# Kernel tuning notes

Measured on AMD Instinct MI355X. Metric: run time of the kernel, lower is better.

The kernel has to match this reference:

```python
import jax, jax.numpy as jnp
import numpy as np

B, S, E, F = 64, 8192, 8, 32  # batch, seq, embed_dim(=n_qubits), ffn_dim


def setup_inputs() -> dict:
    key = jax.random.key(0)
    k_x, k_t, k_w1, k_b1, k_w2, k_b2 = jax.random.split(key, 6)
    x = jax.random.normal(k_x, (B, S, E), dtype=jnp.float32)
    theta = jax.random.normal(k_t, (E,), dtype=jnp.float32)  # trainable RX angles
    lim1 = 1.0 / np.sqrt(E)
    lim2 = 1.0 / np.sqrt(F)
    w1 = jax.random.uniform(k_w1, (E, F), jnp.float32, -lim1, lim1)
    b1 = jax.random.uniform(k_b1, (F,), jnp.float32, -lim1, lim1)
    w2 = jax.random.uniform(k_w2, (F, E), jnp.float32, -lim2, lim2)
    b2 = jax.random.uniform(k_b2, (E,), jnp.float32, -lim2, lim2)
    return {"x": x, "theta": theta, "w1": w1, "b1": b1, "w2": w2, "b2": b2}


def reference(x, theta, w1, b1, w2, b2):
    # Quantum circuit: per wire i, RX(x_i) then RX(theta_i) on |0>, measure PauliZ.
    # Single-qubit RX gates compose: <Z> after RX(phi)|0> = cos(phi). Wires are
    # independent (no entangling gates), so MeasureAll(PauliZ) = cos(x + theta).
    q_out = jnp.cos(x + theta)                      # [B, S, E]
    h = jax.nn.relu(q_out @ w1 + b1)                # [B, S, F]
    return h @ w2 + b2                              # [B, S, E]
```

## Files before the change

kernel.cpp:

```cpp
#include <hip/hip_runtime.h>


#define TPB 256

typedef _Float16 h8  __attribute__((ext_vector_type(8)));
typedef __fp16   fp16x2 __attribute__((ext_vector_type(2)));
typedef float    f4  __attribute__((ext_vector_type(4)));
typedef float    f16v __attribute__((ext_vector_type(16)));

union H2I { fp16x2 h; int i; };
union I4H8 { int i[4]; h8 h; };

__device__ __forceinline__ int pack_f16(float a, float b) {
    H2I u;
    u.h = __builtin_amdgcn_cvt_pkrtz(a, b);
    return u.i;
}

__global__ __launch_bounds__(TPB) void ffq_kernel(
    const float4* __restrict__ xv,
    const float*  __restrict__ theta,
    const float*  __restrict__ w1,
    const float*  __restrict__ b1,
    const float*  __restrict__ w2,
    const float*  __restrict__ b2,
    float4*       __restrict__ outv,
    int ntile, int nwaves)
{
    __shared__ int lds[4 * 576];

    const int tid  = threadIdx.x;
    const int lane = tid & 63;
    const int widx = tid >> 6;
    const int half = lane >> 5;
    const int l31  = lane & 31;
    const int quad = (lane >> 4) & 3;
    const int m16  = lane & 15;

    h8 a1;
#pragma unroll
    for (int j = 0; j < 8; ++j)
        a1[j] = (half == 0) ? (_Float16)w1[j * 32 + l31] : (_Float16)0;

    h8 a2;
#pragma unroll
    for (int j = 0; j < 8; ++j)
        a2[j] = (m16 < 8) ? (_Float16)w2[(quad * 8 + j) * 8 + m16] : (_Float16)0;

    f16v c10;
#pragma unroll
    for (int r = 0; r < 16; ++r)
        c10[r] = b1[(r & 3) + 8 * (r >> 2) + 4 * half];

    f4 c20;
#pragma unroll
    for (int r = 0; r < 4; ++r)
        c20[r] = (quad < 2) ? b2[quad * 4 + r] : 0.0f;

    float th[8];
#pragma unroll
    for (int e = 0; e < 8; ++e) th[e] = theta[e];

    const int base_w = widx * 576;
    const int wid = blockIdx.x * (TPB / 64) + widx;

    float4 curA = make_float4(0.f, 0.f, 0.f, 0.f);
    float4 curC = curA;
    if (wid < ntile && half == 0) {
        const int tok = wid * 32 + l31;
        curA = xv[2 * tok];
        curC = xv[2 * tok + 1];
    }

    for (int tile = wid; tile < ntile; tile += nwaves) {
        float4 nA = curA, nC = curC;
        const int nxt = tile + nwaves;
        if (nxt < ntile && half == 0) {
            const int tok = nxt * 32 + l31;
            nA = xv[2 * tok];
            nC = xv[2 * tok + 1];
        }

        h8 bq;
#pragma unroll
        for (int j = 0; j < 8; ++j) bq[j] = (_Float16)0;
        if (half == 0) {
            bq[0] = (_Float16)__cosf(curA.x + th[0]);
            bq[1] = (_Float16)__cosf(curA.y + th[1]);
            bq[2] = (_Float16)__cosf(curA.z + th[2]);
            bq[3] = (_Float16)__cosf(curA.w + th[3]);
            bq[4] = (_Float16)__cosf(curC.x + th[4]);
            bq[5] = (_Float16)__cosf(curC.y + th[5]);
            bq[6] = (_Float16)__cosf(curC.z + th[6]);
            bq[7] = (_Float16)__cosf(curC.w + th[7]);
        }

        f16v c1 = __builtin_amdgcn_mfma_f32_32x32x16_f16(a1, bq, c10, 0, 0, 0);

#pragma unroll
        for (int r = 0; r < 16; ++r) c1[r] = fmaxf(c1[r], 0.0f);
        int pk[8];
#pragma unroll
        for (int i = 0; i < 8; ++i) pk[i] = pack_f16(c1[2 * i], c1[2 * i + 1]);

#pragma unroll
        for (int i = 0; i < 8; ++i)
            lds[base_w + lane * 9 + i] = pk[i];

#pragma unroll
        for (int tg = 0; tg < 2; ++tg) {
            I4H8 bh;
#pragma unroll
            for (int p = 0; p < 4; ++p)
                bh.i[p] = lds[base_w + (32 * (p >> 1) + 16 * tg + m16) * 9
                              + 2 * quad + (p & 1)];

            f4 o = __builtin_amdgcn_mfma_f32_16x16x32_f16(a2, bh.h, c20, 0, 0, 0);

            if (quad < 2) {
                const int tok = tile * 32 + 16 * tg + m16;
                outv[2 * tok + quad] = make_float4(o[0], o[1], o[2], o[3]);
            }
        }

        curA = nA; curC = nC;
    }
}

extern "C" void kernel_launch(void* const* d_in, const int* in_sizes, int n_in,
                              void* d_out, int out_size, void* d_ws, size_t ws_size,
                              hipStream_t stream) {
    const float* x     = (const float*)d_in[0];
    const float* theta = (const float*)d_in[1];
    const float* w1    = (const float*)d_in[2];
    const float* b1    = (const float*)d_in[3];
    const float* w2    = (const float*)d_in[4];
    const float* b2    = (const float*)d_in[5];
    float* out = (float*)d_out;

    const int ntok  = in_sizes[0] / 8;
    const int ntile = ntok / 32;
    const int grid  = 1024;
    const int nwaves = grid * (TPB / 64);

    ffq_kernel<<<grid, TPB, 0, stream>>>(
        (const float4*)x, theta, w1, b1, w2, b2, (float4*)out, ntile, nwaves);
}
```

Measured before the change: 81.13 us.

## Replace LDS transpose with permlane32 swaps and process 64 tokens per wave

Each wave now handles 64 tokens. All lanes load x and compute cos, and the result goes through two layer-1 MFMAs with half-masked B operands. The layer-1 output is moved into layer-2 operand layout with permlane32_swap instead of an LDS write/read round trip, and layer 2 uses two 32x32x16 MFMAs in place of 16x16x32. The launch grid becomes one wave per 64-token pair, which drops the persistent loop and the register double-buffered prefetch. This removes LDS traffic and idle half-waves, at the cost of more MFMA work on zero padding and no explicit load prefetch.

```diff
diff --git a/kernel.cpp b/kernel.cpp
--- a/kernel.cpp
+++ b/kernel.cpp
@@ -5,8 +5,8 @@
 
 typedef _Float16 h8  __attribute__((ext_vector_type(8)));
 typedef __fp16   fp16x2 __attribute__((ext_vector_type(2)));
-typedef float    f4  __attribute__((ext_vector_type(4)));
 typedef float    f16v __attribute__((ext_vector_type(16)));
+typedef int      i2  __attribute__((ext_vector_type(2)));
 
 union H2I { fp16x2 h; int i; };
 union I4H8 { int i[4]; h8 h; };
@@ -17,6 +17,30 @@
     return u.i;
 }
 
+__device__ __forceinline__ void layer2_store(
+    const f16v c1, const h8 a2a, const h8 a2b, const f16v c20,
+    float4* __restrict__ outv, int tok, int halfidx)
+{
+    int pk[8];
+#pragma unroll
+    for (int i = 0; i < 8; ++i)
+        pk[i] = pack_f16(fmaxf(c1[2 * i], 0.0f), fmaxf(c1[2 * i + 1], 0.0f));
+
+    i2 s0 = __builtin_amdgcn_permlane32_swap(pk[0], pk[2], false, false);
+    i2 s1 = __builtin_amdgcn_permlane32_swap(pk[1], pk[3], false, false);
+    i2 s2 = __builtin_amdgcn_permlane32_swap(pk[4], pk[6], false, false);
+    i2 s3 = __builtin_amdgcn_permlane32_swap(pk[5], pk[7], false, false);
+
+    I4H8 ba, bb;
+    ba.i[0] = s0.x; ba.i[1] = s1.x; ba.i[2] = s0.y; ba.i[3] = s1.y;
+    bb.i[0] = s2.x; bb.i[1] = s3.x; bb.i[2] = s2.y; bb.i[3] = s3.y;
+
+    f16v o = __builtin_amdgcn_mfma_f32_32x32x16_f16(a2a, ba.h, c20, 0, 0, 0);
+    o      = __builtin_amdgcn_mfma_f32_32x32x16_f16(a2b, bb.h, o,   0, 0, 0);
+
+    outv[2 * tok + halfidx] = make_float4(o[0], o[1], o[2], o[3]);
+}
+
 __global__ __launch_bounds__(TPB) void ffq_kernel(
     const float4* __restrict__ xv,
     const float*  __restrict__ theta,
@@ -25,105 +49,74 @@
     const float*  __restrict__ w2,
     const float*  __restrict__ b2,
     float4*       __restrict__ outv,
-    int ntile, int nwaves)
+    int npair, int nwaves)
 {
-    __shared__ int lds[4 * 576];
-
     const int tid  = threadIdx.x;
     const int lane = tid & 63;
-    const int widx = tid >> 6;
     const int half = lane >> 5;
     const int l31  = lane & 31;
-    const int quad = (lane >> 4) & 3;
-    const int m16  = lane & 15;
 
     h8 a1;
 #pragma unroll
     for (int j = 0; j < 8; ++j)
-        a1[j] = (half == 0) ? (_Float16)w1[j * 32 + l31] : (_Float16)0;
+        a1[j] = (_Float16)w1[j * 32 + l31];
 
-    h8 a2;
+    h8 a2a, a2b;
 #pragma unroll
-    for (int j = 0; j < 8; ++j)
-        a2[j] = (m16 < 8) ? (_Float16)w2[(quad * 8 + j) * 8 + m16] : (_Float16)0;
+    for (int j = 0; j < 8; ++j) {
+        a2a[j] = (l31 < 8) ? (_Float16)w2[(8 * half + j) * 8 + l31]      : (_Float16)0;
+        a2b[j] = (l31 < 8) ? (_Float16)w2[(16 + 8 * half + j) * 8 + l31] : (_Float16)0;
+    }
 
     f16v c10;
 #pragma unroll
-    for (int r = 0; r < 16; ++r)
-        c10[r] = b1[(r & 3) + 8 * (r >> 2) + 4 * half];
+    for (int g = 0; g < 4; ++g) {
+        const float4 v = ((const float4*)b1)[2 * g + half];
+        c10[4 * g + 0] = v.x; c10[4 * g + 1] = v.y;
+        c10[4 * g + 2] = v.z; c10[4 * g + 3] = v.w;
+    }
 
-    f4 c20;
+    f16v c20;
 #pragma unroll
-    for (int r = 0; r < 4; ++r)
-        c20[r] = (quad < 2) ? b2[quad * 4 + r] : 0.0f;
+    for (int r = 0; r < 16; ++r) c20[r] = 0.0f;
+    {
+        const float4 v = ((const float4*)b2)[half];
+        c20[0] = v.x; c20[1] = v.y; c20[2] = v.z; c20[3] = v.w;
+    }
 
     float th[8];
 #pragma unroll
     for (int e = 0; e < 8; ++e) th[e] = theta[e];
 
-    const int base_w = widx * 576;
-    const int wid = blockIdx.x * (TPB / 64) + widx;
+    const int wid = blockIdx.x * (TPB / 64) + (tid >> 6);
 
-    float4 curA = make_float4(0.f, 0.f, 0.f, 0.f);
-    float4 curC = curA;
-    if (wid < ntile && half == 0) {
-        const int tok = wid * 32 + l31;
-        curA = xv[2 * tok];
-        curC = xv[2 * tok + 1];
-    }
+    for (int pair = wid; pair < npair; pair += nwaves) {
+        const int tok = pair * 64 + lane;
+        const float4 xa = xv[2 * tok];
+        const float4 xb = xv[2 * tok + 1];
 
-    for (int tile = wid; tile < ntile; tile += nwaves) {
-        float4 nA = curA, nC = curC;
-        const int nxt = tile + nwaves;
-        if (nxt < ntile && half == 0) {
-            const int tok = nxt * 32 + l31;
-            nA = xv[2 * tok];
-            nC = xv[2 * tok + 1];
+        I4H8 q;
+        q.h[0] = (_Float16)__cosf(xa.x + th[0]);
+        q.h[1] = (_Float16)__cosf(xa.y + th[1]);
+        q.h[2] = (_Float16)__cosf(xa.z + th[2]);
+        q.h[3] = (_Float16)__cosf(xa.w + th[3]);
+        q.h[4] = (_Float16)__cosf(xb.x + th[4]);
+        q.h[5] = (_Float16)__cosf(xb.y + th[5]);
+        q.h[6] = (_Float16)__cosf(xb.z + th[6]);
+        q.h[7] = (_Float16)__cosf(xb.w + th[7]);
+
+        I4H8 b0, b1q;
+#pragma unroll
+        for (int p = 0; p < 4; ++p) {
+            b0.i[p]  = half ? 0 : q.i[p];
+            b1q.i[p] = half ? q.i[p] : 0;
         }
 
-        h8 bq;
-#pragma unroll
-        for (int j = 0; j < 8; ++j) bq[j] = (_Float16)0;
-        if (half == 0) {
-            bq[0] = (_Float16)__cosf(curA.x + th[0]);
-            bq[1] = (_Float16)__cosf(curA.y + th[1]);
-            bq[2] = (_Float16)__cosf(curA.z + th[2]);
-            bq[3] = (_Float16)__cosf(curA.w + th[3]);
-            bq[4] = (_Float16)__cosf(curC.x + th[4]);
-            bq[5] = (_Float16)__cosf(curC.y + th[5]);
-            bq[6] = (_Float16)__cosf(curC.z + th[6]);
-            bq[7] = (_Float16)__cosf(curC.w + th[7]);
-        }
+        const f16v c1_0 = __builtin_amdgcn_mfma_f32_32x32x16_f16(a1, b0.h,  c10, 0, 0, 0);
+        const f16v c1_1 = __builtin_amdgcn_mfma_f32_32x32x16_f16(a1, b1q.h, c10, 0, 0, 0);
 
-        f16v c1 = __builtin_amdgcn_mfma_f32_32x32x16_f16(a1, bq, c10, 0, 0, 0);
-
-#pragma unroll
-        for (int r = 0; r < 16; ++r) c1[r] = fmaxf(c1[r], 0.0f);
-        int pk[8];
-#pragma unroll
-        for (int i = 0; i < 8; ++i) pk[i] = pack_f16(c1[2 * i], c1[2 * i + 1]);
-
-#pragma unroll
-        for (int i = 0; i < 8; ++i)
-            lds[base_w + lane * 9 + i] = pk[i];
-
-#pragma unroll
-        for (int tg = 0; tg < 2; ++tg) {
-            I4H8 bh;
-#pragma unroll
-            for (int p = 0; p < 4; ++p)
-                bh.i[p] = lds[base_w + (32 * (p >> 1) + 16 * tg + m16) * 9
-                              + 2 * quad + (p & 1)];
-
-            f4 o = __builtin_amdgcn_mfma_f32_16x16x32_f16(a2, bh.h, c20, 0, 0, 0);
-
-            if (quad < 2) {
-                const int tok = tile * 32 + 16 * tg + m16;
-                outv[2 * tok + quad] = make_float4(o[0], o[1], o[2], o[3]);
-            }
-        }
-
-        curA = nA; curC = nC;
+        layer2_store(c1_0, a2a, a2b, c20, outv, pair * 64 + l31,      half);
+        layer2_store(c1_1, a2a, a2b, c20, outv, pair * 64 + 32 + l31, half);
     }
 }
 
@@ -139,10 +132,11 @@
     float* out = (float*)d_out;
 
     const int ntok  = in_sizes[0] / 8;
-    const int ntile = ntok / 32;
-    const int grid  = 1024;
-    const int nwaves = grid * (TPB / 64);
+    const int npair = ntok / 64;
+    const int wpb   = TPB / 64;
+    const int grid  = (npair + wpb - 1) / wpb;
+    const int nwaves = grid * wpb;
 
     ffq_kernel<<<grid, TPB, 0, stream>>>(
-        (const float4*)x, theta, w1, b1, w2, b2, (float4*)out, ntile, nwaves);
+        (const float4*)x, theta, w1, b1, w2, b2, (float4*)out, npair, nwaves);
 }
```

Result: no change. 80.44 us (-0.8%).
